# Kernel tuning notes

Hardware: AMD Instinct MI355X
Metric: run time of the kernel (lower is better)

Reference implementation:

```python
import jax, jax.numpy as jnp
import numpy as np
from jax import lax

N = 100_000      # active voxels
C = 64           # nIn == nOut
K = 343          # 7*7*7 depthwise taps
HID = 4 * C      # pointwise expansion
EPS = 1e-5
CENTER = K // 2  # self offset


def setup_inputs() -> dict:
    key = jax.random.key(0)
    ks = jax.random.split(key, 10)
    x_feat = jax.random.normal(ks[0], (N, C), dtype=jnp.float32)
    nbr = jax.random.randint(ks[1], (N, K), 0, N, dtype=jnp.int32)
    valid = jax.random.uniform(ks[2], (N, K)) < 0.25
    nbr = jnp.where(valid, nbr, jnp.int32(N))
    nbr = nbr.at[:, CENTER].set(jnp.arange(N, dtype=jnp.int32))  # submanifold: center is self
    W1 = jax.random.normal(ks[3], (K, C), dtype=jnp.float32) * 0.05
    b1 = jax.random.normal(ks[4], (C,), dtype=jnp.float32) * 0.02
    gamma = jnp.ones((C,), dtype=jnp.float32)
    beta = jnp.zeros((C,), dtype=jnp.float32)
    W2 = jax.random.normal(ks[5], (C, HID), dtype=jnp.float32) * (1.0 / np.sqrt(C))
    b2 = jax.random.normal(ks[6], (HID,), dtype=jnp.float32) * 0.02
    W3 = jax.random.normal(ks[7], (HID, C), dtype=jnp.float32) * (1.0 / np.sqrt(HID))
    b3 = jax.random.normal(ks[8], (C,), dtype=jnp.float32) * 0.02
    return {"x_feat": x_feat, "nbr_idx": nbr, "W1": W1, "b1": b1,
            "gamma": gamma, "beta": beta, "W2": W2, "b2": b2, "W3": W3, "b3": b3}


def _depthwise_submanifold(feat, nbr_idx, W1, b1):
    # feat [N,C]; nbr_idx [N,K] with sentinel N -> zero contribution
    feat_pad = jnp.concatenate([feat, jnp.zeros((1, feat.shape[1]), feat.dtype)], axis=0)
    def step(acc, xs):
        idx_k, w_k = xs                       # [N], [C]
        return acc + feat_pad[idx_k] * w_k, None  # gather + per-channel MAC
    acc0 = jnp.zeros_like(feat)
    out, _ = lax.scan(step, acc0, (nbr_idx.T, W1))  # scan over K=343 taps
    return out + b1


def _groupnorm1(h, gamma, beta):
    # num_groups=1 over channels, per active site
    mu = jnp.mean(h, axis=-1, keepdims=True)
    var = jnp.var(h, axis=-1, keepdims=True)
    return (h - mu) * lax.rsqrt(var + EPS) * gamma + beta


def reference(x_feat, nbr_idx, W1, b1, gamma, beta, W2, b2, W3, b3):
    h = _depthwise_submanifold(x_feat, nbr_idx, W1, b1)  # conv1 (depthwise 7^3)
    h = _groupnorm1(h, gamma, beta)                      # norm
    h = h @ W2 + b2                                      # conv2 (1x1x1, C->4C)
    h = jax.nn.gelu(h, approximate=False)                # exact GELU (torch default)
    h = h @ W3 + b3                                      # conv3 (1x1x1, 4C->C)
    return h + x_feat                                    # residual add
```

## Files before the change

kernel.cpp:

```cpp
#include <hip/hip_runtime.h>
#include <hip/hip_fp16.h>
#include <math.h>

#define CH    64
#define KT    343
#define HIDD  256
#define KCAP  144

typedef __attribute__((ext_vector_type(8))) _Float16 half8;
typedef __attribute__((ext_vector_type(4))) _Float16 half4;
typedef __attribute__((ext_vector_type(4))) float f32x4;
struct H24 { __half2 x, y, z, w; };

#define MEMBAR() asm volatile("" ::: "memory")

__global__ __launch_bounds__(256) void prep_kernel(
    const float* __restrict__ W1, const float* __restrict__ W2,
    const float* __restrict__ W3, const float* __restrict__ x,
    _Float16* __restrict__ W1h, _Float16* __restrict__ W2Th,
    _Float16* __restrict__ W3Th, _Float16* __restrict__ xh, int nelem) {
  const int t = blockIdx.x * 256 + threadIdx.x;
  const int step = gridDim.x * 256;
  for (int e = t; e < KT * CH; e += step) W1h[e] = (_Float16)W1[e];
  for (int e = t; e < CH * HIDD; e += step) {
    int k = e >> 8, n = e & 255;
    W2Th[n * CH + k] = (_Float16)W2[e];
  }
  for (int e = t; e < HIDD * CH; e += step) {
    int k = e >> 6, n = e & 63;
    W3Th[n * HIDD + k] = (_Float16)W3[e];
  }
  const int tot4 = nelem / 4 + 16;
  for (int q = t; q < tot4; q += step) {
    const int eb = q * 4;
    float4 v = (eb < nelem) ? *(const float4*)(x + eb) : make_float4(0.f, 0.f, 0.f, 0.f);
    half4 o;
    o[0] = (_Float16)v.x; o[1] = (_Float16)v.y;
    o[2] = (_Float16)v.z; o[3] = (_Float16)v.w;
    *(half4*)(xh + eb) = o;
  }
}

__global__ __launch_bounds__(256) void compact_kernel(
    const int* __restrict__ nbr, int* __restrict__ packed,
    int* __restrict__ cnt, int N) {
  const int w = (blockIdx.x * 256 + threadIdx.x) >> 6;
  const int lane = threadIdx.x & 63;
  if (w >= N) return;
  const int* row = nbr + (size_t)w * KT;
  int* prow = packed + (size_t)w * KCAP;
  int base = 0;
#pragma unroll
  for (int p = 0; p < 6; ++p) {
    const int tap = p * 64 + lane;
    const int idx = (tap < KT) ? row[tap] : N;
    const bool valid = (tap < KT) && (idx != N);
    const unsigned long long mask = __ballot(valid);
    const int pos = __popcll(mask & ((1ull << lane) - 1ull));
    if (valid) {
      const int wp = base + pos;
      if (wp < KCAP) prow[wp] = idx | (tap << 17);
    }
    base += __popcll(mask);
  }
  if (lane == 0) cnt[w] = (base < KCAP) ? base : KCAP;
}

#define ISSUE8(buf, pkb, vi)                                                \
  { _Pragma("unroll") for (int p = 0; p < 8; ++p) {                         \
      const int pk_ = __builtin_amdgcn_ds_bpermute(pb + 4 * p, (vi));       \
      pkb[p] = pk_;                                                         \
      buf[p] = *(const uint4*)(xb + ((((unsigned)pk_ & 0x1FFFFu) << 7) + (unsigned)e16)); } }

#define CONSUME8(buf, pkb)                                                  \
  { _Pragma("unroll") for (int p = 0; p < 8; ++p) {                         \
      const uint4 wq_ = *(const uint4*)&W1s[((((unsigned)pkb[p]) >> 17) << 7) + e16]; \
      const H24 gh_ = __builtin_bit_cast(H24, buf[p]);                      \
      const H24 wh_ = __builtin_bit_cast(H24, wq_);                         \
      acc0 = __hfma2(gh_.x, wh_.x, acc0);                                   \
      acc1 = __hfma2(gh_.y, wh_.y, acc1);                                   \
      acc2 = __hfma2(gh_.z, wh_.z, acc2);                                   \
      acc3 = __hfma2(gh_.w, wh_.w, acc3); } }

__global__ __launch_bounds__(256, 3) void fused_kernel(
    const _Float16* __restrict__ xh, const float* __restrict__ x,
    const int* __restrict__ packed, const int* __restrict__ cnt,
    const float* __restrict__ b1, const float* __restrict__ gamma,
    const float* __restrict__ beta, const _Float16* __restrict__ W2Th,
    const float* __restrict__ b2, const _Float16* __restrict__ W3Th,
    const float* __restrict__ b3, float* __restrict__ out, int N) {
  __shared__ __align__(16) char W1s[43904];
  __shared__ __align__(16) _Float16 hs[32][CH + 8];
  _Float16 (*gs)[HIDD + 8] = (_Float16 (*)[HIDD + 8])W1s;

  const int t = threadIdx.x;
  const int wvid = t >> 6;
  const int lane = t & 63;
  const int g = lane >> 3;
  const int e = lane & 7;
  const int e16 = e << 4;
  const int pb = (lane & 56) << 2;
  const int vbase = blockIdx.x * 32;
  const int vb = __builtin_amdgcn_readfirstlane(vbase + wvid * 8);

  {
    const uint4* src = (const uint4*)W2Th;
  }
  {
    const uint4* src = (const uint4*)((const char*)W2Th - 0);
  }
  {
    extern __shared__ char _dummy[];
  }
  {
    const uint4* src = (const uint4*)( (const void*)0 );
    (void)src;
  }
  {
    const _Float16* W1h = (const _Float16*)nullptr; (void)W1h;
  }
  {
  }

  {
    const size_t xh_elems = ((size_t)(N + 1) * CH * 2 + 255) & ~(size_t)255;
    const uint4* src = (const uint4*)((const char*)xh + xh_elems);
    uint4* dst = (uint4*)W1s;
    for (int q = t; q < 2744; q += 256) dst[q] = src[q];
  }

  const int cnt_g = cnt[vb + g];
  int mx = cnt_g;
  mx = max(mx, __shfl_xor(mx, 8));
  mx = max(mx, __shfl_xor(mx, 16));
  mx = max(mx, __shfl_xor(mx, 32));
  const int nck2 = __builtin_amdgcn_readfirstlane((((mx + 7) >> 3) + 1) & ~1);
  const int* prow = packed + (size_t)(vb + g) * KCAP;
  const int PADV = N;
  const char* xb = (const char*)xh;

  __half2 acc0 = __float2half2_rn(0.f), acc1 = acc0, acc2 = acc0, acc3 = acc0;

  uint4 ga[8], gb[8];
  int pka[8], pkb2[8];

  #define LDE(ck) ( (((ck) * 8 + e) < cnt_g) ? prow[(ck) * 8 + e] : PADV )

  int viA = LDE(0);
  int viB = LDE(1);
  ISSUE8(ga, pka, viA);
  __syncthreads();

  for (int ck = 0; ck < nck2; ck += 2) {
    const int viC = (ck + 2 < nck2) ? LDE(ck + 2) : PADV;
    MEMBAR();
    ISSUE8(gb, pkb2, viB);
    MEMBAR();
    CONSUME8(ga, pka);
    const int viD = (ck + 3 < nck2) ? LDE(ck + 3) : PADV;
    MEMBAR();
    if (ck + 2 < nck2) ISSUE8(ga, pka, viC);
    MEMBAR();
    CONSUME8(gb, pkb2);
    viB = viD;
  }

  float fa[8];
  fa[0] = __low2float(acc0); fa[1] = __high2float(acc0);
  fa[2] = __low2float(acc1); fa[3] = __high2float(acc1);
  fa[4] = __low2float(acc2); fa[5] = __high2float(acc2);
  fa[6] = __low2float(acc3); fa[7] = __high2float(acc3);
  {
    float4 blo = *(const float4*)(b1 + e * 8);
    float4 bhi = *(const float4*)(b1 + e * 8 + 4);
    fa[0] += blo.x; fa[1] += blo.y; fa[2] += blo.z; fa[3] += blo.w;
    fa[4] += bhi.x; fa[5] += bhi.y; fa[6] += bhi.z; fa[7] += bhi.w;
  }
  float s = 0.f, ss = 0.f;
#pragma unroll
  for (int d = 0; d < 8; ++d) { s += fa[d]; ss += fa[d] * fa[d]; }
  s += __shfl_xor(s, 1); ss += __shfl_xor(ss, 1);
  s += __shfl_xor(s, 2); ss += __shfl_xor(ss, 2);
  s += __shfl_xor(s, 4); ss += __shfl_xor(ss, 4);
  const float mu = s * (1.0f / 64.0f);
  const float var = ss * (1.0f / 64.0f) - mu * mu;
  const float inv = rsqrtf(var + 1e-5f);
  {
    float4 glo = *(const float4*)(gamma + e * 8);
    float4 ghi = *(const float4*)(gamma + e * 8 + 4);
    float4 tlo = *(const float4*)(beta + e * 8);
    float4 thi = *(const float4*)(beta + e * 8 + 4);
    const float gm[8] = {glo.x, glo.y, glo.z, glo.w, ghi.x, ghi.y, ghi.z, ghi.w};
    const float bt[8] = {tlo.x, tlo.y, tlo.z, tlo.w, thi.x, thi.y, thi.z, thi.w};
    half8 hv;
#pragma unroll
    for (int d = 0; d < 8; ++d)
      hv[d] = (_Float16)((fa[d] - mu) * inv * gm[d] + bt[d]);
    *(half8*)&hs[wvid * 8 + g][e * 8] = hv;
  }
  __syncthreads();

  const int row16 = lane & 15, quad = lane >> 4;
  half8 afr[2][2];
#pragma unroll
  for (int rt = 0; rt < 2; ++rt)
#pragma unroll
    for (int ks = 0; ks < 2; ++ks)
      afr[rt][ks] = *(const half8*)&hs[rt * 16 + row16][ks * 32 + quad * 8];

#pragma unroll
  for (int cl = 0; cl < 4; ++cl) {
    const int n = wvid * 64 + cl * 16 + row16;
    f32x4 a0 = {0.f, 0.f, 0.f, 0.f}, a1 = {0.f, 0.f, 0.f, 0.f};
#pragma unroll
    for (int ks = 0; ks < 2; ++ks) {
      half8 bfr = *(const half8*)(W2Th + (size_t)n * CH + ks * 32 + quad * 8);
      a0 = __builtin_amdgcn_mfma_f32_16x16x32_f16(afr[0][ks], bfr, a0, 0, 0, 0);
      a1 = __builtin_amdgcn_mfma_f32_16x16x32_f16(afr[1][ks], bfr, a1, 0, 0, 0);
    }
    const float bias = b2[n];
#pragma unroll
    for (int r = 0; r < 4; ++r) {
      float z0 = a0[r] + bias;
      float z1 = a1[r] + bias;
      gs[quad * 4 + r][n]      = (_Float16)(0.5f * z0 * (1.0f + erff(z0 * 0.70710678118654752f)));
      gs[16 + quad * 4 + r][n] = (_Float16)(0.5f * z1 * (1.0f + erff(z1 * 0.70710678118654752f)));
    }
  }
  __syncthreads();

  f32x4 o0 = {0.f, 0.f, 0.f, 0.f}, o1 = {0.f, 0.f, 0.f, 0.f};
  const int oc = wvid * 16 + row16;
#pragma unroll
  for (int ks = 0; ks < 8; ++ks) {
    half8 bfr = *(const half8*)(W3Th + (size_t)oc * HIDD + ks * 32 + quad * 8);
    half8 a20 = *(const half8*)&gs[row16][ks * 32 + quad * 8];
    half8 a21 = *(const half8*)&gs[16 + row16][ks * 32 + quad * 8];
    o0 = __builtin_amdgcn_mfma_f32_16x16x32_f16(a20, bfr, o0, 0, 0, 0);
    o1 = __builtin_amdgcn_mfma_f32_16x16x32_f16(a21, bfr, o1, 0, 0, 0);
  }
  const float bias3 = b3[oc];
#pragma unroll
  for (int r = 0; r < 4; ++r) {
    size_t v0 = (size_t)vbase + quad * 4 + r;
    size_t v1 = (size_t)vbase + 16 + quad * 4 + r;
    out[v0 * CH + oc] = o0[r] + bias3 + x[v0 * CH + oc];
    out[v1 * CH + oc] = o1[r] + bias3 + x[v1 * CH + oc];
  }
}

extern "C" void kernel_launch(void* const* d_in, const int* in_sizes, int n_in,
                              void* d_out, int out_size, void* d_ws, size_t ws_size,
                              hipStream_t stream) {
  const float* x_feat = (const float*)d_in[0];
  const int*   nbr    = (const int*)d_in[1];
  const float* W1     = (const float*)d_in[2];
  const float* b1     = (const float*)d_in[3];
  const float* gamma  = (const float*)d_in[4];
  const float* beta   = (const float*)d_in[5];
  const float* W2     = (const float*)d_in[6];
  const float* b2     = (const float*)d_in[7];
  const float* W3     = (const float*)d_in[8];
  const float* b3     = (const float*)d_in[9];
  float* out = (float*)d_out;

  const int N = in_sizes[0] / CH;

  char* ws = (char*)d_ws;
  size_t off = 0;
  _Float16* xh = (_Float16*)(ws + off);
  off += (((size_t)(N + 1) * CH * 2) + 255) & ~(size_t)255;
  _Float16* W1h = (_Float16*)(ws + off);
  off += ((size_t)KT * CH * 2 + 255) & ~(size_t)255;
  _Float16* W2Th = (_Float16*)(ws + off);
  off += ((size_t)HIDD * CH * 2 + 255) & ~(size_t)255;
  _Float16* W3Th = (_Float16*)(ws + off);
  off += ((size_t)CH * HIDD * 2 + 255) & ~(size_t)255;
  int* packed = (int*)(ws + off);
  off += ((size_t)N * KCAP * 4 + 255) & ~(size_t)255;
  int* cnt = (int*)(ws + off);
  off += ((size_t)N * 4 + 255) & ~(size_t)255;

  hipLaunchKernelGGL(prep_kernel, dim3(1024), dim3(256), 0, stream,
                     W1, W2, W3, x_feat, W1h, W2Th, W3Th, xh, N * CH);
  hipLaunchKernelGGL(compact_kernel, dim3((N + 3) / 4), dim3(256), 0, stream,
                     nbr, packed, cnt, N);
  hipLaunchKernelGGL(fused_kernel, dim3(N / 32), dim3(256), 0, stream,
                     xh, x_feat, packed, cnt, b1, gamma, beta,
                     W2Th, b2, W3Th, b3, out, N);
}
```

Before: 409.4 us.

## Fuse prep and compaction kernels, double block size of fused kernel

```diff
diff --git a/kernel.cpp b/kernel.cpp
--- a/kernel.cpp
+++ b/kernel.cpp
@@ -14,11 +14,19 @@
 
 #define MEMBAR() asm volatile("" ::: "memory")
 
-__global__ __launch_bounds__(256) void prep_kernel(
+#define PRELOAD6(v, w)                                                     \
+  { const int* row_ = nbr + (size_t)(w) * KT;                              \
+    _Pragma("unroll") for (int p = 0; p < 6; ++p) {                        \
+      const int tap_ = p * 64 + lane;                                      \
+      v[p] = (tap_ < KT) ? row_[tap_] : N; } }
+
+__global__ __launch_bounds__(256) void prep_compact_kernel(
     const float* __restrict__ W1, const float* __restrict__ W2,
     const float* __restrict__ W3, const float* __restrict__ x,
-    _Float16* __restrict__ W1h, _Float16* __restrict__ W2Th,
-    _Float16* __restrict__ W3Th, _Float16* __restrict__ xh, int nelem) {
+    const int* __restrict__ nbr, _Float16* __restrict__ W1h,
+    _Float16* __restrict__ W2Th, _Float16* __restrict__ W3Th,
+    _Float16* __restrict__ xh, int* __restrict__ packed,
+    int* __restrict__ cnt, int N, int nelem) {
   const int t = blockIdx.x * 256 + threadIdx.x;
   const int step = gridDim.x * 256;
   for (int e = t; e < KT * CH; e += step) W1h[e] = (_Float16)W1[e];
@@ -39,31 +47,38 @@
     o[2] = (_Float16)v.z; o[3] = (_Float16)v.w;
     *(half4*)(xh + eb) = o;
   }
-}
-
-__global__ __launch_bounds__(256) void compact_kernel(
-    const int* __restrict__ nbr, int* __restrict__ packed,
-    int* __restrict__ cnt, int N) {
-  const int w = (blockIdx.x * 256 + threadIdx.x) >> 6;
+
   const int lane = threadIdx.x & 63;
-  if (w >= N) return;
-  const int* row = nbr + (size_t)w * KT;
-  int* prow = packed + (size_t)w * KCAP;
-  int base = 0;
-#pragma unroll
-  for (int p = 0; p < 6; ++p) {
-    const int tap = p * 64 + lane;
-    const int idx = (tap < KT) ? row[tap] : N;
-    const bool valid = (tap < KT) && (idx != N);
-    const unsigned long long mask = __ballot(valid);
-    const int pos = __popcll(mask & ((1ull << lane) - 1ull));
-    if (valid) {
-      const int wp = base + pos;
-      if (wp < KCAP) prow[wp] = idx | (tap << 17);
+  const int wv = t >> 6;
+  const int nw = (gridDim.x * 256) >> 6;
+  int w = wv;
+  if (w < N) {
+    int v[6];
+    PRELOAD6(v, w);
+    while (w < N) {
+      const int wn = w + nw;
+      int vn[6];
+      if (wn < N) PRELOAD6(vn, wn);
+      int* prow = packed + (size_t)w * KCAP;
+      int base = 0;
+#pragma unroll
+      for (int p = 0; p < 6; ++p) {
+        const int tap = p * 64 + lane;
+        const bool valid = (tap < KT) && (v[p] != N);
+        const unsigned long long m = __ballot(valid);
+        const int pos = __popcll(m & ((1ull << lane) - 1ull));
+        if (valid) {
+          const int wp = base + pos;
+          if (wp < KCAP) prow[wp] = v[p] | (tap << 17);
+        }
+        base += __popcll(m);
+      }
+      if (lane == 0) cnt[w] = (base < KCAP) ? base : KCAP;
+      w = wn;
+#pragma unroll
+      for (int p = 0; p < 6; ++p) v[p] = vn[p];
     }
-    base += __popcll(mask);
-  }
-  if (lane == 0) cnt[w] = (base < KCAP) ? base : KCAP;
+  }
 }
 
 #define ISSUE8(buf, pkb, vi)                                                \
@@ -82,15 +97,16 @@
       acc2 = __hfma2(gh_.z, wh_.z, acc2);                                   \
       acc3 = __hfma2(gh_.w, wh_.w, acc3); } }
 
-__global__ __launch_bounds__(256, 3) void fused_kernel(
+__global__ __launch_bounds__(512, 6) void fused_kernel(
     const _Float16* __restrict__ xh, const float* __restrict__ x,
     const int* __restrict__ packed, const int* __restrict__ cnt,
+    const _Float16* __restrict__ W1h,
     const float* __restrict__ b1, const float* __restrict__ gamma,
     const float* __restrict__ beta, const _Float16* __restrict__ W2Th,
     const float* __restrict__ b2, const _Float16* __restrict__ W3Th,
     const float* __restrict__ b3, float* __restrict__ out, int N) {
   __shared__ __align__(16) char W1s[43904];
-  __shared__ __align__(16) _Float16 hs[32][CH + 8];
+  __shared__ __align__(16) _Float16 hs[64][CH + 8];
   _Float16 (*gs)[HIDD + 8] = (_Float16 (*)[HIDD + 8])W1s;
 
   const int t = threadIdx.x;
@@ -100,33 +116,13 @@
   const int e = lane & 7;
   const int e16 = e << 4;
   const int pb = (lane & 56) << 2;
-  const int vbase = blockIdx.x * 32;
-  const int vb = __builtin_amdgcn_readfirstlane(vbase + wvid * 8);
+  const int vbase = blockIdx.x * 64;
+  const int vb = __builtin_amdgcn_readfirstlane(min(vbase + wvid * 8, N - 8));
 
   {
-    const uint4* src = (const uint4*)W2Th;
-  }
-  {
-    const uint4* src = (const uint4*)((const char*)W2Th - 0);
-  }
-  {
-    extern __shared__ char _dummy[];
-  }
-  {
-    const uint4* src = (const uint4*)( (const void*)0 );
-    (void)src;
-  }
-  {
-    const _Float16* W1h = (const _Float16*)nullptr; (void)W1h;
-  }
-  {
-  }
-
-  {
-    const size_t xh_elems = ((size_t)(N + 1) * CH * 2 + 255) & ~(size_t)255;
-    const uint4* src = (const uint4*)((const char*)xh + xh_elems);
+    const uint4* src = (const uint4*)W1h;
     uint4* dst = (uint4*)W1s;
-    for (int q = t; q < 2744; q += 256) dst[q] = src[q];
+    for (int q = t; q < 2744; q += 512) dst[q] = src[q];
   }
 
   const int cnt_g = cnt[vb + g];
@@ -201,16 +197,17 @@
   __syncthreads();
 
   const int row16 = lane & 15, quad = lane >> 4;
+  const int rh = wvid >> 2, wc = wvid & 3;
   half8 afr[2][2];
 #pragma unroll
   for (int rt = 0; rt < 2; ++rt)
 #pragma unroll
     for (int ks = 0; ks < 2; ++ks)
-      afr[rt][ks] = *(const half8*)&hs[rt * 16 + row16][ks * 32 + quad * 8];
+      afr[rt][ks] = *(const half8*)&hs[rh * 32 + rt * 16 + row16][ks * 32 + quad * 8];
 
 #pragma unroll
   for (int cl = 0; cl < 4; ++cl) {
-    const int n = wvid * 64 + cl * 16 + row16;
+    const int n = wc * 64 + cl * 16 + row16;
     f32x4 a0 = {0.f, 0.f, 0.f, 0.f}, a1 = {0.f, 0.f, 0.f, 0.f};
 #pragma unroll
     for (int ks = 0; ks < 2; ++ks) {
@@ -223,29 +220,29 @@
     for (int r = 0; r < 4; ++r) {
       float z0 = a0[r] + bias;
       float z1 = a1[r] + bias;
-      gs[quad * 4 + r][n]      = (_Float16)(0.5f * z0 * (1.0f + erff(z0 * 0.70710678118654752f)));
-      gs[16 + quad * 4 + r][n] = (_Float16)(0.5f * z1 * (1.0f + erff(z1 * 0.70710678118654752f)));
+      gs[rh * 32 + quad * 4 + r][n]      = (_Float16)(0.5f * z0 * (1.0f + erff(z0 * 0.70710678118654752f)));
+      gs[rh * 32 + 16 + quad * 4 + r][n] = (_Float16)(0.5f * z1 * (1.0f + erff(z1 * 0.70710678118654752f)));
     }
   }
   __syncthreads();
 
   f32x4 o0 = {0.f, 0.f, 0.f, 0.f}, o1 = {0.f, 0.f, 0.f, 0.f};
-  const int oc = wvid * 16 + row16;
+  const int oc = wc * 16 + row16;
 #pragma unroll
   for (int ks = 0; ks < 8; ++ks) {
     half8 bfr = *(const half8*)(W3Th + (size_t)oc * HIDD + ks * 32 + quad * 8);
-    half8 a20 = *(const half8*)&gs[row16][ks * 32 + quad * 8];
-    half8 a21 = *(const half8*)&gs[16 + row16][ks * 32 + quad * 8];
+    half8 a20 = *(const half8*)&gs[rh * 32 + row16][ks * 32 + quad * 8];
+    half8 a21 = *(const half8*)&gs[rh * 32 + 16 + row16][ks * 32 + quad * 8];
     o0 = __builtin_amdgcn_mfma_f32_16x16x32_f16(a20, bfr, o0, 0, 0, 0);
     o1 = __builtin_amdgcn_mfma_f32_16x16x32_f16(a21, bfr, o1, 0, 0, 0);
   }
   const float bias3 = b3[oc];
 #pragma unroll
   for (int r = 0; r < 4; ++r) {
-    size_t v0 = (size_t)vbase + quad * 4 + r;
-    size_t v1 = (size_t)vbase + 16 + quad * 4 + r;
-    out[v0 * CH + oc] = o0[r] + bias3 + x[v0 * CH + oc];
-    out[v1 * CH + oc] = o1[r] + bias3 + x[v1 * CH + oc];
+    const int v0 = vbase + rh * 32 + quad * 4 + r;
+    const int v1 = vbase + rh * 32 + 16 + quad * 4 + r;
+    if (v0 < N) out[(size_t)v0 * CH + oc] = o0[r] + bias3 + x[(size_t)v0 * CH + oc];
+    if (v1 < N) out[(size_t)v1 * CH + oc] = o1[r] + bias3 + x[(size_t)v1 * CH + oc];
   }
 }
 
@@ -281,11 +278,10 @@
   int* cnt = (int*)(ws + off);
   off += ((size_t)N * 4 + 255) & ~(size_t)255;
 
-  hipLaunchKernelGGL(prep_kernel, dim3(1024), dim3(256), 0, stream,
-                     W1, W2, W3, x_feat, W1h, W2Th, W3Th, xh, N * CH);
-  hipLaunchKernelGGL(compact_kernel, dim3((N + 3) / 4), dim3(256), 0, stream,
-                     nbr, packed, cnt, N);
-  hipLaunchKernelGGL(fused_kernel, dim3(N / 32), dim3(256), 0, stream,
-                     xh, x_feat, packed, cnt, b1, gamma, beta,
+  hipLaunchKernelGGL(prep_compact_kernel, dim3(2048), dim3(256), 0, stream,
+                     W1, W2, W3, x_feat, nbr, W1h, W2Th, W3Th, xh,
+                     packed, cnt, N, N * CH);
+  hipLaunchKernelGGL(fused_kernel, dim3((N + 63) / 64), dim3(512), 0, stream,
+                     xh, x_feat, packed, cnt, W1h, b1, gamma, beta,
                      W2Th, b2, W3Th, b3, out, N);
 }
```

After: 1.020 ms. 2.49x slower.
